# Performance work log

Measured on AMD Instinct MI355X. Metric: run time of the kernel, lower is better.

## Reference

```python
import jax, jax.numpy as jnp
import numpy as np
from math import sqrt

B, S, E, H = 4, 2048, 1024, 16
DH = E // H  # 64


def setup_inputs() -> dict:
    key = jax.random.key(0)
    ks = jax.random.split(key, 10)
    sc = 0.02
    return {
        "x": jax.random.normal(ks[0], (B, S, E), dtype=jnp.float32),
        # per-head projection weights stacked: [H, E, DH], biases [H, DH]
        "Wq": jax.random.normal(ks[1], (H, E, DH), dtype=jnp.float32) * sc,
        "bq": jax.random.normal(ks[2], (H, DH), dtype=jnp.float32) * sc,
        "Wk": jax.random.normal(ks[3], (H, E, DH), dtype=jnp.float32) * sc,
        "bk": jax.random.normal(ks[4], (H, DH), dtype=jnp.float32) * sc,
        "Wv": jax.random.normal(ks[5], (H, E, DH), dtype=jnp.float32) * sc,
        "bv": jax.random.normal(ks[6], (H, DH), dtype=jnp.float32) * sc,
        "Wo": jax.random.normal(ks[7], (E, E), dtype=jnp.float32) * sc,
        "bo": jax.random.normal(ks[8], (E,), dtype=jnp.float32) * sc,
    }


def reference(x, Wq, bq, Wk, bk, Wv, bv, Wo, bo):
    # Batched QKV projections (equivalent to the per-head Linear loop)
    q = jnp.einsum("bse,hed->bhsd", x, Wq) + bq[None, :, None, :]
    k = jnp.einsum("bse,hed->bhsd", x, Wk) + bk[None, :, None, :]
    v = jnp.einsum("bse,hed->bhsd", x, Wv) + bv[None, :, None, :]
    scores = jnp.einsum("bhsd,bhtd->bhst", q, k) / sqrt(DH)
    # masked=False in the module, so plain softmax over keys
    weights = jax.nn.softmax(scores, axis=-1)
    attn = jnp.einsum("bhst,bhtd->bhsd", weights, v)
    # concat heads: [B,S,H*DH] with head i contiguous (matches torch.cat dim=-1)
    concat = attn.transpose(0, 2, 1, 3).reshape(B, S, H * DH)
    out = concat @ Wo.T if Wo.shape == (E, E) and False else jnp.einsum("bsf,ef->bse", concat, Wo) + bo
    return out
```

## Files before the change

### kernel.cpp

```cpp
#include <hip/hip_runtime.h>
#include <math.h>

#define Bc 4
#define Sc 2048
#define Ec 1024
#define Hc 16
#define DHc 64

typedef unsigned short u16;
typedef __attribute__((ext_vector_type(8))) short short8;
typedef __attribute__((ext_vector_type(4))) float f32x4;
typedef __attribute__((ext_vector_type(16))) float f32x16;
typedef __attribute__((ext_vector_type(2))) unsigned short u16x2;

union pk8 { unsigned int u[4]; short8 v; };

__device__ __forceinline__ u16 f2bf(float f) {
    unsigned int u = __float_as_uint(f);
    u += 0x7FFFu + ((u >> 16) & 1u);
    return (u16)(u >> 16);
}

__device__ __forceinline__ void gl_lds16(const void* g, void* l) {
    __builtin_amdgcn_global_load_lds(
        (const __attribute__((address_space(1))) unsigned int*)g,
        (__attribute__((address_space(3))) unsigned int*)l,
        16, 0, 0);
}

__global__ __launch_bounds__(256)
void prep_kernel(const float* __restrict__ x,
                 const float* __restrict__ Wq, const float* __restrict__ Wk,
                 const float* __restrict__ Wv, const float* __restrict__ Wo,
                 u16* __restrict__ xb, u16* __restrict__ Wob, u16* __restrict__ Wtb)
{
    __shared__ float T[64][65];
    const int bid = blockIdx.x;
    const int t = threadIdx.x;

    if (bid < 4096 + 512) {
        const float* src = (bid < 4096) ? x : Wo;
        u16* dst = (bid < 4096) ? xb : Wob;
        size_t i = (size_t)(bid < 4096 ? bid : bid - 4096) * 256 + t;
        const float* p = src + i * 8;
        float4 a = *(const float4*)p;
        float4 b = *(const float4*)(p + 4);
        short8 v;
        v[0] = (short)f2bf(a.x); v[1] = (short)f2bf(a.y);
        v[2] = (short)f2bf(a.z); v[3] = (short)f2bf(a.w);
        v[4] = (short)f2bf(b.x); v[5] = (short)f2bf(b.y);
        v[6] = (short)f2bf(b.z); v[7] = (short)f2bf(b.w);
        *(short8*)(dst + i * 8) = v;
        return;
    }

    const int bid2 = bid - 4608;
    const int proj = bid2 >> 8;
    const int h = (bid2 >> 4) & 15;
    const int e0 = (bid2 & 15) * 64;
    const float* W = (proj == 0) ? Wq : (proj == 1) ? Wk : Wv;

    #pragma unroll
    for (int i = 0; i < 4; ++i) {
        int fid = t + i * 256;
        int row = fid >> 4, c4 = fid & 15;
        float4 v = *(const float4*)(W + ((size_t)h * Ec + e0 + row) * DHc + c4 * 4);
        T[row][c4 * 4 + 0] = v.x; T[row][c4 * 4 + 1] = v.y;
        T[row][c4 * 4 + 2] = v.z; T[row][c4 * 4 + 3] = v.w;
    }
    __syncthreads();
    const int d = t >> 2, ech = (t & 3) * 16;
    u16* dst = Wtb + ((size_t)(proj * Hc + h) * DHc + d) * Ec + e0 + ech;
    #pragma unroll
    for (int j = 0; j < 16; j += 2) {
        u16x2 v2;
        v2.x = f2bf(T[ech + j][d]);
        v2.y = f2bf(T[ech + j + 1][d]);
        *(u16x2*)(dst + j) = v2;
    }
}

__global__ __launch_bounds__(256)
void qkv_mfma_kernel(const u16* __restrict__ xb, const u16* __restrict__ Wtb,
                     const float* __restrict__ bq, const float* __restrict__ bk,
                     const float* __restrict__ bv,
                     u16* __restrict__ qb, u16* __restrict__ kb, u16* __restrict__ vb)
{
    __shared__ __align__(16) u16 As[128 * 64];
    __shared__ __align__(16) u16 Bs[128 * 64];

    const int t = threadIdx.x;
    const int w = t >> 6, l = t & 63;
    const int wr = w >> 1, wc = w & 1;
    const int id = blockIdx.x;
    const int j = id >> 3;
    const int mBase = ((id & 7) * 8 + (j & 7)) * 128;
    const int nBase = (j >> 3) * 128;
    const int proj = nBase >> 10;
    const int nIn = nBase & (Ec - 1);
    const int lr = l >> 3, ls = l & 7;
    const int lq = l >> 4, ln = l & 15;

    f32x4 acc[4][4];
    #pragma unroll
    for (int i = 0; i < 4; ++i)
        #pragma unroll
        for (int jj = 0; jj < 4; ++jj) acc[i][jj] = (f32x4)0.f;

    for (int k0 = 0; k0 < Ec; k0 += 64) {
        __syncthreads();
        #pragma unroll
        for (int c = 0; c < 8; ++c) {
            int cg = w * 8 + c;
            if (cg < 16) {
                int row = cg * 8 + lr;
                int g = ls ^ (row & 7);
                gl_lds16(xb + ((size_t)(mBase + row)) * Ec + k0 + g * 8,
                         (void*)(As + cg * 512));
            } else {
                int col = (cg - 16) * 8 + lr;
                int g = ls ^ (col & 7);
                gl_lds16(Wtb + ((size_t)proj * Ec + nIn + col) * Ec + k0 + g * 8,
                         (void*)(Bs + (cg - 16) * 512));
            }
        }
        __syncthreads();

        #pragma unroll
        for (int ks = 0; ks < 2; ++ks) {
            short8 af[4], bfr[4];
            int gg = ks * 4 + lq;
            #pragma unroll
            for (int fm = 0; fm < 4; ++fm) {
                int row = wr * 64 + fm * 16 + ln;
                af[fm] = *(const short8*)(As + row * 64 + ((gg ^ (row & 7)) * 8));
            }
            #pragma unroll
            for (int fn = 0; fn < 4; ++fn) {
                int col = wc * 64 + fn * 16 + ln;
                bfr[fn] = *(const short8*)(Bs + col * 64 + ((gg ^ (col & 7)) * 8));
            }
            #pragma unroll
            for (int fm = 0; fm < 4; ++fm)
                #pragma unroll
                for (int fn = 0; fn < 4; ++fn)
                    acc[fm][fn] = __builtin_amdgcn_mfma_f32_16x16x32_bf16(
                        af[fm], bfr[fn], acc[fm][fn], 0, 0, 0);
        }
    }

    const float* bias = (proj == 0) ? bq : (proj == 1) ? bk : bv;
    #pragma unroll
    for (int fn = 0; fn < 4; ++fn) {
        int n = nBase + wc * 64 + fn * 16 + ln;
        int cc = n & (Ec - 1);
        int hh = cc >> 6, d = cc & 63;
        float bv_ = bias[cc];
        #pragma unroll
        for (int fm = 0; fm < 4; ++fm) {
            #pragma unroll
            for (int r = 0; r < 4; ++r) {
                int m = mBase + wr * 64 + fm * 16 + lq * 4 + r;
                int b = m >> 11, s = m & (Sc - 1);
                int bh = b * Hc + hh;
                float vv = acc[fm][fn][r] + bv_;
                if (proj == 0)      qb[((size_t)bh * Sc + s) * DHc + d] = f2bf(vv * 0.18033688011f);
                else if (proj == 1) kb[((size_t)bh * Sc + s) * DHc + d] = f2bf(vv);
                else                vb[((size_t)bh * DHc + d) * Sc + s] = f2bf(vv);
            }
        }
    }
}

__global__ __launch_bounds__(512, 4)
void attn_mfma_kernel(const u16* __restrict__ qb, const u16* __restrict__ kb,
                      const u16* __restrict__ vb, u16* __restrict__ concatb)
{
    __shared__ __align__(16) u16 Kt[2][64 * 64];
    __shared__ __align__(16) u16 Vt[2][64 * 64];

    const int t = threadIdx.x;
    const int w = t >> 6, l = t & 63;
    const int id = blockIdx.x;
    const int j = id >> 3;
    const int qt = j >> 3;
    const int hb = (id & 7) * 8 + (j & 7);
    const int h = hb & 15, b = hb >> 4;
    const int bh = b * Hc + h;
    const int hi = l >> 5, l5 = l & 31;
    const int lr = l >> 3, ls = l & 7;
    const int sw5 = l5 & 7;

    const u16* qp = qb + ((size_t)bh * Sc + qt * 256 + w * 32 + l5) * DHc;
    const u16* kp = kb + (size_t)bh * Sc * DHc;
    const u16* vp = vb + (size_t)bh * DHc * Sc;

    const int cg = w * 2;

    short8 qf[4];
    #pragma unroll
    for (int ks = 0; ks < 4; ++ks)
        qf[ks] = *(const short8*)(qp + ks * 16 + hi * 8);

    f32x16 o0 = (f32x16)0.f, o1 = (f32x16)0.f;
    float l_i = 0.f;

    #pragma unroll
    for (int c = 0; c < 2; ++c) {
        int g2 = cg + c;
        if (g2 < 8) {
            int row = g2 * 8 + lr;
            int g = ls ^ (row & 7);
            gl_lds16(kp + ((size_t)row) * DHc + g * 8, (void*)(Kt[0] + g2 * 512));
        } else {
            int d = (g2 - 8) * 8 + lr;
            int g = ls ^ (d & 7);
            gl_lds16(vp + (size_t)d * Sc + g * 8, (void*)(Vt[0] + (g2 - 8) * 512));
        }
    }
    asm volatile("s_waitcnt vmcnt(0)" ::: "memory");
    __syncthreads();

    for (int kt = 0; kt < Sc / 64; ++kt) {
        const int cur = kt & 1;
        if (kt + 1 < Sc / 64) {
            const int nxt = cur ^ 1;
            #pragma unroll
            for (int c = 0; c < 2; ++c) {
                int g2 = cg + c;
                if (g2 < 8) {
                    int row = g2 * 8 + lr;
                    int g = ls ^ (row & 7);
                    gl_lds16(kp + ((size_t)((kt + 1) * 64 + row)) * DHc + g * 8,
                             (void*)(Kt[nxt] + g2 * 512));
                } else {
                    int d = (g2 - 8) * 8 + lr;
                    int g = ls ^ (d & 7);
                    gl_lds16(vp + (size_t)d * Sc + (kt + 1) * 64 + g * 8,
                             (void*)(Vt[nxt] + (g2 - 8) * 512));
                }
            }
        }

        f32x16 s0 = (f32x16)0.f, s1 = (f32x16)0.f;
        __builtin_amdgcn_s_setprio(1);
        #pragma unroll
        for (int ks = 0; ks < 4; ++ks) {
            int slot = ((2 * ks + hi) ^ sw5) * 8;
            short8 kf0 = *(const short8*)(Kt[cur] + (l5) * 64 + slot);
            short8 kf1 = *(const short8*)(Kt[cur] + (32 + l5) * 64 + slot);
            s0 = __builtin_amdgcn_mfma_f32_32x32x16_bf16(kf0, qf[ks], s0, 0, 0, 0);
            s1 = __builtin_amdgcn_mfma_f32_32x32x16_bf16(kf1, qf[ks], s1, 0, 0, 0);
        }
        __builtin_amdgcn_s_setprio(0);

        float sum = 0.f;

#define PROC_KG(SV, KG)                                                         \
        {                                                                       \
            float p_[16];                                                       \
            _Pragma("unroll")                                                   \
            for (int r = 0; r < 16; ++r) {                                      \
                p_[r] = exp2f(SV[r] - 16.0f);                                   \
                sum += p_[r];                                                   \
            }                                                                   \
            unsigned int W_[8];                                                 \
            _Pragma("unroll")                                                   \
            for (int i = 0; i < 8; ++i)                                         \
                asm("v_cvt_pk_bf16_f32 %0, %1, %2"                              \
                    : "=v"(W_[i]) : "v"(p_[2 * i]), "v"(p_[2 * i + 1]));        \
            unsigned int r0 = __shfl_xor(hi ? W_[0] : W_[2], 32);               \
            unsigned int r1 = __shfl_xor(hi ? W_[1] : W_[3], 32);               \
            unsigned int r2 = __shfl_xor(hi ? W_[4] : W_[6], 32);               \
            unsigned int r3 = __shfl_xor(hi ? W_[5] : W_[7], 32);               \
            pk8 a0, a1;                                                         \
            a0.u[0] = hi ? r0 : W_[0];  a0.u[1] = hi ? r1 : W_[1];              \
            a0.u[2] = hi ? W_[2] : r0;  a0.u[3] = hi ? W_[3] : r1;              \
            a1.u[0] = hi ? r2 : W_[4];  a1.u[1] = hi ? r3 : W_[5];              \
            a1.u[2] = hi ? W_[6] : r2;  a1.u[3] = hi ? W_[7] : r3;              \
            _Pragma("unroll")                                                   \
            for (int ksl = 0; ksl < 2; ++ksl) {                                 \
                int slot = (((KG * 4 + ksl * 2 + hi)) ^ sw5) * 8;               \
                short8 vf0 = *(const short8*)(Vt[cur] + (l5) * 64 + slot);      \
                short8 vf1 = *(const short8*)(Vt[cur] + (32 + l5) * 64 + slot); \
                short8 pa = ksl ? a1.v : a0.v;                                  \
                o0 = __builtin_amdgcn_mfma_f32_32x32x16_bf16(pa, vf0, o0, 0, 0, 0); \
                o1 = __builtin_amdgcn_mfma_f32_32x32x16_bf16(pa, vf1, o1, 0, 0, 0); \
            }                                                                   \
        }

        __builtin_amdgcn_s_setprio(1);
        PROC_KG(s0, 0)
        PROC_KG(s1, 1)
        __builtin_amdgcn_s_setprio(0);
#undef PROC_KG

        sum += __shfl_xor(sum, 32);
        l_i += sum;

        asm volatile("s_waitcnt vmcnt(0)" ::: "memory");
        __syncthreads();
    }

    #pragma unroll
    for (int r = 0; r < 16; ++r) {
        int qrow = (r & 3) + 8 * (r >> 2) + 4 * hi;
        float inv = 1.f / __shfl(l_i, qrow);
        int q = qt * 256 + w * 32 + qrow;
        u16* dst = concatb + ((size_t)b * Sc + q) * Ec + h * DHc + l5;
        dst[0]  = f2bf(o0[r] * inv);
        dst[32] = f2bf(o1[r] * inv);
    }
}

__global__ __launch_bounds__(256)
void oproj_mfma_kernel(const u16* __restrict__ cb, const u16* __restrict__ Wob,
                       const float* __restrict__ bo, float* __restrict__ out)
{
    __shared__ __align__(16) u16 As[128 * 64];
    __shared__ __align__(16) u16 Bs[128 * 64];

    const int t = threadIdx.x;
    const int w = t >> 6, l = t & 63;
    const int wr = w >> 1, wc = w & 1;
    const int id = blockIdx.x;
    const int j = id >> 3;
    const int mBase = ((id & 7) * 8 + (j & 7)) * 128;
    const int nBase = (j >> 3) * 128;
    const int lr = l >> 3, ls = l & 7;
    const int lq = l >> 4, ln = l & 15;

    f32x4 acc[4][4];
    #pragma unroll
    for (int i = 0; i < 4; ++i)
        #pragma unroll
        for (int jj = 0; jj < 4; ++jj) acc[i][jj] = (f32x4)0.f;

    for (int k0 = 0; k0 < Ec; k0 += 64) {
        __syncthreads();
        #pragma unroll
        for (int c = 0; c < 8; ++c) {
            int cg = w * 8 + c;
            if (cg < 16) {
                int row = cg * 8 + lr;
                int g = ls ^ (row & 7);
                gl_lds16(cb + ((size_t)(mBase + row)) * Ec + k0 + g * 8,
                         (void*)(As + cg * 512));
            } else {
                int col = (cg - 16) * 8 + lr;
                int g = ls ^ (col & 7);
                gl_lds16(Wob + ((size_t)(nBase + col)) * Ec + k0 + g * 8,
                         (void*)(Bs + (cg - 16) * 512));
            }
        }
        __syncthreads();

        #pragma unroll
        for (int ks = 0; ks < 2; ++ks) {
            short8 af[4], bfr[4];
            int gg = ks * 4 + lq;
            #pragma unroll
            for (int fm = 0; fm < 4; ++fm) {
                int row = wr * 64 + fm * 16 + ln;
                af[fm] = *(const short8*)(As + row * 64 + ((gg ^ (row & 7)) * 8));
            }
            #pragma unroll
            for (int fn = 0; fn < 4; ++fn) {
                int col = wc * 64 + fn * 16 + ln;
                bfr[fn] = *(const short8*)(Bs + col * 64 + ((gg ^ (col & 7)) * 8));
            }
            #pragma unroll
            for (int fm = 0; fm < 4; ++fm)
                #pragma unroll
                for (int fn = 0; fn < 4; ++fn)
                    acc[fm][fn] = __builtin_amdgcn_mfma_f32_16x16x32_bf16(
                        af[fm], bfr[fn], acc[fm][fn], 0, 0, 0);
        }
    }

    #pragma unroll
    for (int fn = 0; fn < 4; ++fn) {
        int n = nBase + wc * 64 + fn * 16 + ln;
        float bb = bo[n];
        #pragma unroll
        for (int fm = 0; fm < 4; ++fm) {
            #pragma unroll
            for (int r = 0; r < 4; ++r) {
                int m = mBase + wr * 64 + fm * 16 + lq * 4 + r;
                out[(size_t)m * Ec + n] = acc[fm][fn][r] + bb;
            }
        }
    }
}

extern "C" void kernel_launch(void* const* d_in, const int* in_sizes, int n_in,
                              void* d_out, int out_size, void* d_ws, size_t ws_size,
                              hipStream_t stream)
{
    const float* x  = (const float*)d_in[0];
    const float* Wq = (const float*)d_in[1];
    const float* bq = (const float*)d_in[2];
    const float* Wk = (const float*)d_in[3];
    const float* bk = (const float*)d_in[4];
    const float* Wv = (const float*)d_in[5];
    const float* bv = (const float*)d_in[6];
    const float* Wo = (const float*)d_in[7];
    const float* bo = (const float*)d_in[8];
    float* out = (float*)d_out;

    char* ws = (char*)d_ws;
    u16* xb   = (u16*)(ws);
    u16* Wtb  = (u16*)(ws + (16u << 20));
    u16* Wob  = (u16*)(ws + (22u << 20));
    u16* qbuf = (u16*)(ws + (24u << 20));
    u16* kbuf = (u16*)(ws + (40u << 20));
    u16* vbuf = (u16*)(ws + (56u << 20));
    u16* cbuf = (u16*)(ws + (72u << 20));

    prep_kernel<<<dim3(5376, 1, 1), 256, 0, stream>>>(x, Wq, Wk, Wv, Wo, xb, Wob, Wtb);

    qkv_mfma_kernel<<<dim3(1536, 1, 1), 256, 0, stream>>>(xb, Wtb, bq, bk, bv, qbuf, kbuf, vbuf);

    attn_mfma_kernel<<<dim3(512, 1, 1), 512, 0, stream>>>(qbuf, kbuf, vbuf, cbuf);

    oproj_mfma_kernel<<<dim3(512, 1, 1), 256, 0, stream>>>(cbuf, Wob, bo, out);
}
```

Baseline: 225.6 us.

## Split attention over two key halves and merge partials in a combine kernel

The attention kernel now splits the key/value sequence into two halves, doubling the grid from 512 to 1024 blocks. Each block writes unnormalized bf16 partial outputs and per-row softmax sums to scratch buffers, reusing the workspace regions of x and the transposed weights. A new elementwise combine kernel adds the two partials and divides by the summed denominators before the output projection. The aim is more resident waves per CU for better latency hiding, at the cost of extra global memory traffic, one more launch, and added bf16 rounding on the partials.

```diff
diff --git a/kernel.cpp b/kernel.cpp
--- a/kernel.cpp
+++ b/kernel.cpp
@@ -19,6 +19,10 @@
     unsigned int u = __float_as_uint(f);
     u += 0x7FFFu + ((u >> 16) & 1u);
     return (u16)(u >> 16);
+}
+
+__device__ __forceinline__ float bf2f(short s) {
+    return __uint_as_float(((unsigned int)(u16)s) << 16);
 }
 
 __device__ __forceinline__ void gl_lds16(const void* g, void* l) {
@@ -174,7 +178,9 @@
 
 __global__ __launch_bounds__(512, 4)
 void attn_mfma_kernel(const u16* __restrict__ qb, const u16* __restrict__ kb,
-                      const u16* __restrict__ vb, u16* __restrict__ concatb)
+                      const u16* __restrict__ vb,
+                      u16* __restrict__ pA, u16* __restrict__ pB,
+                      float* __restrict__ lbuf)
 {
     __shared__ __align__(16) u16 Kt[2][64 * 64];
     __shared__ __align__(16) u16 Vt[2][64 * 64];
@@ -183,14 +189,17 @@
     const int w = t >> 6, l = t & 63;
     const int id = blockIdx.x;
     const int j = id >> 3;
-    const int qt = j >> 3;
     const int hb = (id & 7) * 8 + (j & 7);
+    const int qt = (j >> 3) & 7;
+    const int split = j >> 6;
     const int h = hb & 15, b = hb >> 4;
     const int bh = b * Hc + h;
     const int hi = l >> 5, l5 = l & 31;
     const int lr = l >> 3, ls = l & 7;
     const int sw5 = l5 & 7;
 
+    const int kt0 = split * 16;
+
     const u16* qp = qb + ((size_t)bh * Sc + qt * 256 + w * 32 + l5) * DHc;
     const u16* kp = kb + (size_t)bh * Sc * DHc;
     const u16* vp = vb + (size_t)bh * DHc * Sc;
@@ -211,19 +220,19 @@
         if (g2 < 8) {
             int row = g2 * 8 + lr;
             int g = ls ^ (row & 7);
-            gl_lds16(kp + ((size_t)row) * DHc + g * 8, (void*)(Kt[0] + g2 * 512));
+            gl_lds16(kp + ((size_t)(kt0 * 64 + row)) * DHc + g * 8, (void*)(Kt[0] + g2 * 512));
         } else {
             int d = (g2 - 8) * 8 + lr;
             int g = ls ^ (d & 7);
-            gl_lds16(vp + (size_t)d * Sc + g * 8, (void*)(Vt[0] + (g2 - 8) * 512));
+            gl_lds16(vp + (size_t)d * Sc + kt0 * 64 + g * 8, (void*)(Vt[0] + (g2 - 8) * 512));
         }
     }
     asm volatile("s_waitcnt vmcnt(0)" ::: "memory");
     __syncthreads();
 
-    for (int kt = 0; kt < Sc / 64; ++kt) {
+    for (int kt = kt0; kt < kt0 + 16; ++kt) {
         const int cur = kt & 1;
-        if (kt + 1 < Sc / 64) {
+        if (kt + 1 < kt0 + 16) {
             const int nxt = cur ^ 1;
             #pragma unroll
             for (int c = 0; c < 2; ++c) {
@@ -302,15 +311,41 @@
         __syncthreads();
     }
 
+    u16* pbuf = split ? pB : pA;
     #pragma unroll
     for (int r = 0; r < 16; ++r) {
         int qrow = (r & 3) + 8 * (r >> 2) + 4 * hi;
-        float inv = 1.f / __shfl(l_i, qrow);
         int q = qt * 256 + w * 32 + qrow;
-        u16* dst = concatb + ((size_t)b * Sc + q) * Ec + h * DHc + l5;
-        dst[0]  = f2bf(o0[r] * inv);
-        dst[32] = f2bf(o1[r] * inv);
-    }
+        u16* dst = pbuf + ((size_t)b * Sc + q) * Ec + h * DHc + l5;
+        dst[0]  = f2bf(o0[r]);
+        dst[32] = f2bf(o1[r]);
+    }
+    if (l < 32) {
+        int q = qt * 256 + w * 32 + l5;
+        lbuf[((size_t)split * 64 + bh) * Sc + q] = l_i;
+    }
+}
+
+__global__ __launch_bounds__(256)
+void combine_kernel(const u16* __restrict__ pA, const u16* __restrict__ pB,
+                    const float* __restrict__ lbuf, u16* __restrict__ outb)
+{
+    size_t idx = (size_t)blockIdx.x * 256 + threadIdx.x;
+    size_t flat = idx * 8;
+    int e = (int)(flat & (Ec - 1));
+    int s = (int)((flat >> 10) & (Sc - 1));
+    int b = (int)(flat >> 21);
+    int bh = b * Hc + (e >> 6);
+    float l0 = lbuf[(size_t)bh * Sc + s];
+    float l1 = lbuf[((size_t)64 + bh) * Sc + s];
+    float inv = 1.f / (l0 + l1);
+    short8 a = *(const short8*)(pA + flat);
+    short8 bb = *(const short8*)(pB + flat);
+    short8 o;
+    #pragma unroll
+    for (int j2 = 0; j2 < 8; ++j2)
+        o[j2] = (short)f2bf((bf2f(a[j2]) + bf2f(bb[j2])) * inv);
+    *(short8*)(outb + flat) = o;
 }
 
 __global__ __launch_bounds__(256)
@@ -416,12 +451,16 @@
     u16* kbuf = (u16*)(ws + (40u << 20));
     u16* vbuf = (u16*)(ws + (56u << 20));
     u16* cbuf = (u16*)(ws + (72u << 20));
+    float* lb = (float*)(ws + (16u << 20));
 
     prep_kernel<<<dim3(5376, 1, 1), 256, 0, stream>>>(x, Wq, Wk, Wv, Wo, xb, Wob, Wtb);
 
     qkv_mfma_kernel<<<dim3(1536, 1, 1), 256, 0, stream>>>(xb, Wtb, bq, bk, bv, qbuf, kbuf, vbuf);
 
-    attn_mfma_kernel<<<dim3(512, 1, 1), 512, 0, stream>>>(qbuf, kbuf, vbuf, cbuf);
+    attn_mfma_kernel<<<dim3(1024, 1, 1), 512, 0, stream>>>(qbuf, kbuf, vbuf,
+                                                           cbuf, xb, lb);
+
+    combine_kernel<<<dim3(4096, 1, 1), 256, 0, stream>>>(cbuf, xb, lb, cbuf);
 
     oproj_mfma_kernel<<<dim3(512, 1, 1), 256, 0, stream>>>(cbuf, Wob, bo, out);
 }
```

New measurement: 231.6 us. 2.7% more time.
